# Kernel tuning notes

Measured on AMD Instinct MI355X. Metric: run time of the kernel, lower is better.

The kernel has to match this reference:

```python
import jax, jax.numpy as jnp
import numpy as np

T, B, N, IN, H, K, L = 24, 64, 207, 2, 64, 2, 2


def setup_inputs() -> dict:
    key = jax.random.key(0)
    ks = jax.random.split(key, 12)
    inputs = jax.random.normal(ks[0], (T, B, N, IN), dtype=jnp.float32)
    initial_hidden_state = jnp.zeros((L, B, N * H), dtype=jnp.float32)
    # random row-normalized support (keeps diffusion stable over the scan)
    S = jax.random.uniform(ks[1], (1, N, N), dtype=jnp.float32)
    supports = S / jnp.sum(S, axis=-1, keepdims=True)
    scale = 0.1
    return {
        "inputs": inputs,
        "initial_hidden_state": initial_hidden_state,
        "supports": supports,
        "w_gate0": scale * jax.random.normal(ks[2], ((IN + H) * (K + 1), 2 * H), dtype=jnp.float32),
        "b_gate0": jnp.ones((2 * H,), dtype=jnp.float32),
        "w_cand0": scale * jax.random.normal(ks[3], ((IN + H) * (K + 1), H), dtype=jnp.float32),
        "b_cand0": jnp.zeros((H,), dtype=jnp.float32),
        "w_gate1": scale * jax.random.normal(ks[4], ((H + H) * (K + 1), 2 * H), dtype=jnp.float32),
        "b_gate1": jnp.ones((2 * H,), dtype=jnp.float32),
        "w_cand1": scale * jax.random.normal(ks[5], ((H + H) * (K + 1), H), dtype=jnp.float32),
        "b_cand1": jnp.zeros((H,), dtype=jnp.float32),
    }


def _gconv(supports, x, w, b):
    # x: [B, N, D]; Chebyshev diffusion: x0, x1 = S@x0, x_k = 2*S@x_{k-1} - x_{k-2}
    xs = [x]
    for s in range(supports.shape[0]):
        S = supports[s]
        xk_1 = jnp.einsum('nm,bmd->bnd', S, x)
        xs.append(xk_1)
        xk_2 = x
        for _ in range(2, K + 1):
            xk = 2.0 * jnp.einsum('nm,bmd->bnd', S, xk_1) - xk_2
            xs.append(xk)
            xk_2, xk_1 = xk_1, xk
    h = jnp.concatenate(xs, axis=-1)            # [B, N, D*(K*num_supports+1)]
    return jnp.einsum('bnd,do->bno', h, w) + b


def _cell(supports, x_t, h, wg, bg, wc, bc, in_dim):
    # x_t: [B, N*in_dim], h: [B, N*H]
    bsz = x_t.shape[0]
    x = x_t.reshape(bsz, N, in_dim)
    hh = h.reshape(bsz, N, H)
    gates = jax.nn.sigmoid(_gconv(supports, jnp.concatenate([x, hh], -1), wg, bg))
    r, u = jnp.split(gates, 2, axis=-1)
    c = jnp.tanh(_gconv(supports, jnp.concatenate([x, r * hh], -1), wc, bc))
    h_new = u * hh + (1.0 - u) * c
    return h_new.reshape(bsz, N * H)


def _run_layer(supports, xs, h0, wg, bg, wc, bc, in_dim):
    def step(h, x_t):
        hn = _cell(supports, x_t, h, wg, bg, wc, bc, in_dim)
        return hn, hn
    h_last, outs = jax.lax.scan(step, h0, xs)
    return h_last, outs


def reference(inputs, initial_hidden_state, supports,
              w_gate0, b_gate0, w_cand0, b_cand0,
              w_gate1, b_gate1, w_cand1, b_cand1):
    cur = inputs.reshape(T, inputs.shape[1], -1)          # [T, B, N*IN]
    h0_last, cur = _run_layer(supports, cur, initial_hidden_state[0],
                              w_gate0, b_gate0, w_cand0, b_cand0, IN)
    h1_last, cur = _run_layer(supports, cur, initial_hidden_state[1],
                              w_gate1, b_gate1, w_cand1, b_cand1, H)
    output_hidden = jnp.stack([h0_last, h1_last], axis=0)  # [L, B, N*H]
    return output_hidden, cur                              # cur: [T, B, N*H]
```

## Files before the change

### kernel.cpp

```cpp
#include <hip/hip_runtime.h>
#include <math.h>


typedef unsigned short u16;
typedef unsigned int u32;
typedef short bf8 __attribute__((ext_vector_type(8)));
typedef float f32x4 __attribute__((ext_vector_type(4)));
typedef u16 u16x8 __attribute__((ext_vector_type(8)));

constexpr int T_ = 24, B_ = 64, N_ = 207, H_ = 64;
constexpr int BH  = 4096;
constexpr int NBH = N_ * BH;
constexpr int BNH = B_ * N_ * H_;

__device__ __forceinline__ float b2f(u16 b) {
    u32 u = ((u32)b) << 16; float f; __builtin_memcpy(&f, &u, 4); return f;
}
__device__ __forceinline__ u16 f2b(float f) {
    u32 u; __builtin_memcpy(&u, &f, 4);
    u32 r = (u + 0x7FFF + ((u >> 16) & 1)) >> 16;
    return (u16)r;
}

__global__ void s2_kernel(const float* __restrict__ S, float* __restrict__ S2) {
    const int n = blockIdx.x, m = threadIdx.x;
    if (m >= N_) return;
    float acc = 0.f;
    for (int k = 0; k < N_; ++k) acc += S[n * N_ + k] * S[k * N_ + m];
    S2[n * N_ + m] = 2.f * acc;
}

__global__ void ablk_build(const float* __restrict__ S, const float* __restrict__ S2,
                           u16* __restrict__ ablk) {
    int idx = blockIdx.x * 256 + threadIdx.x;
    if (idx >= 2 * 14 * 7 * 4 * 16 * 8) return;
    int j = idx & 7, r = (idx >> 3) & 15, kb = (idx >> 7) & 3;
    int rest = idx >> 9;
    int ks = rest % 7; rest /= 7;
    int rt = rest % 14, half = rest / 14;
    int n = rt * 16 + r, k = ks * 32 + kb * 8 + j;
    float v = 0.f;
    if (n < N_ && k < N_) v = half ? S2[n * N_ + k] : S[n * N_ + k];
    ablk[idx] = f2b(v);
}

__global__ void wblk_build(const float* __restrict__ W, u16* __restrict__ out,
                           int OF, int total, int layer) {
    int idx = blockIdx.x * 256 + threadIdx.x;
    if (idx >= total) return;
    int j = idx & 7;
    int rest = idx >> 3;
    int o = rest % OF; rest /= OF;
    int kb = rest & 3, ks = rest >> 2;
    int k = ks * 32 + kb * 8 + j;
    int blk = k >> 6, d = k & 63;
    int wrow, wsub = -1;
    if (layer == 0) {
        wrow = blk * 66 + 2 + d;
        if (blk == 0) wsub = 2 * 66 + 2 + d;
    } else {
        int sb = blk >> 1, part = blk & 1;
        wrow = sb * 128 + part * 64 + d;
        if (sb == 0) wsub = 256 + part * 64 + d;
    }
    float v = W[wrow * OF + o];
    if (wsub >= 0) v -= W[wsub * OF + o];
    out[idx] = f2b(v);
}

__global__ void wx_build(const float* __restrict__ W, float* __restrict__ out, int OF) {
    int idx = blockIdx.x * 256 + threadIdx.x;
    if (idx >= 6 * OF) return;
    int o = idx % OF, p = idx / OF;
    int cheb = p >> 1, i = p & 1;
    float v = W[(cheb * 66 + i) * OF + o];
    if (cheb == 0) v -= W[(132 + i) * OF + o];
    out[idx] = v;
}

__global__ void xt2_build(const float* __restrict__ x, u16* __restrict__ xt2) {
    int idx = blockIdx.x * 256 + threadIdx.x;
    if (idx >= N_ * T_ * B_ * 2) return;
    int i = idx & 1, b = (idx >> 1) & 63, rest = idx >> 7;
    int t = rest % T_, n = rest / T_;
    xt2[idx] = f2b(x[((t * B_ + b) * N_ + n) * 2 + i]);
}

__global__ __launch_bounds__(256) void xd_build(const float* __restrict__ S,
                                                const float* __restrict__ S2,
                                                const u16* __restrict__ xt2,
                                                u16* __restrict__ xd0,
                                                u16* __restrict__ xd1) {
    __shared__ float sS[N_], sS2[N_];
    int n = blockIdx.x;
    int c = blockIdx.y * 256 + threadIdx.x;
    for (int i = threadIdx.x; i < N_; i += 256) { sS[i] = S[n*N_+i]; sS2[i] = S2[n*N_+i]; }
    __syncthreads();
    float a1 = 0.f, a2 = 0.f;
    for (int m = 0; m < N_; ++m) {
        float xv = b2f(xt2[m * 3072 + c]);
        a1 += sS[m] * xv; a2 += sS2[m] * xv;
    }
    xd0[(size_t)n * 3072 + c] = f2b(a1);
    xd1[(size_t)n * 3072 + c] = f2b(a2);
}

__global__ void hinit_kernel(const float* __restrict__ ih, u16* __restrict__ h0b,
                             u16* __restrict__ h1b, float* __restrict__ h0f,
                             float* __restrict__ h1f) {
    int idx = blockIdx.x * 256 + threadIdx.x;
    if (idx >= NBH) return;
    int h = idx & 63, b = (idx >> 6) & 63, n = idx >> 12;
    float v0 = ih[(size_t)b * (N_ * 64) + n * 64 + h];
    float v1 = ih[(size_t)BNH + (size_t)b * (N_ * 64) + n * 64 + h];
    h0b[idx] = f2b(v0); h1b[idx] = f2b(v1);
    h0f[idx] = v0;      h1f[idx] = v1;
}

__global__ __launch_bounds__(256) void diff_kernel(
    const u16* __restrict__ ablk,
    const u16* __restrict__ srcA, const u16* __restrict__ srcB, int ctA,
    u16* __restrict__ dA1, u16* __restrict__ dA2,
    u16* __restrict__ dB1, u16* __restrict__ dB2) {
    __shared__ u16 sA[7168];
    __shared__ char sB[28672];
    const int bx = blockIdx.x, by = blockIdx.y;
    const int half = by / 7, rsub = by % 7;
    const int tid = threadIdx.x;
    const u16* src; u16* dst1; u16* dst2; int c0;
    if (bx < ctA) { src = srcA; dst1 = dA1; dst2 = dA2; c0 = bx * 64; }
    else          { src = srcB; dst1 = dB1; dst2 = dB2; c0 = (bx - ctA) * 64; }

    const u16* ga = ablk + (size_t)(half * 14 + rsub * 2) * 3584;
    for (int i = tid; i < 896; i += 256)
        *(u16x8*)(sA + i * 8) = *(const u16x8*)(ga + i * 8);

    for (int id = tid; id < 1792; id += 256) {
        int ks = id >> 8, ch = id & 255;
        int ml = ch >> 3, cc = ch & 7;
        int m = ks * 32 + ml;
        u16x8 v = {0,0,0,0,0,0,0,0};
        if (m < N_) v = *(const u16x8*)(src + (size_t)m * 4096 + c0 + cc * 8);
        *(u16x8*)(sB + ks * 4096 + ((ml * 128 + cc * 16) ^ (((ml >> 3) & 3) << 5))) = v;
    }
    __syncthreads();

    const int w = tid >> 6, lane = tid & 63, lq = lane >> 4, lr = lane & 15;
    const int rt = w & 1, cfb = (w >> 1) * 2;
    f32x4 acc[2] = {{0,0,0,0},{0,0,0,0}};
    for (int ks = 0; ks < 7; ++ks) {
        bf8 a = *(const bf8*)(sA + ((((rt * 7) + ks) * 4 + lq) * 16 + lr) * 8);
#pragma unroll
        for (int cf = 0; cf < 2; ++cf) {
            int c = (cfb + cf) * 16 + lr;
            bf8 b;
#pragma unroll
            for (int j = 0; j < 8; ++j) {
                int m = lq * 8 + j;
                b[j] = *(const short*)(sB + ks * 4096 +
                        ((m * 128 + c * 2) ^ (((m >> 3) & 3) << 5)));
            }
            acc[cf] = __builtin_amdgcn_mfma_f32_16x16x32_bf16(a, b, acc[cf], 0, 0, 0);
        }
    }
    u16* dst = half ? dst2 : dst1;
#pragma unroll
    for (int cf = 0; cf < 2; ++cf) {
        int c = c0 + (cfb + cf) * 16 + lr;
#pragma unroll
        for (int j = 0; j < 4; ++j) {
            int n = rsub * 32 + rt * 16 + lq * 4 + j;
            if (n < N_) dst[(size_t)n * 4096 + c] = f2b(acc[cf][j]);
        }
    }
}

template<int NBLK, int OF, bool XC, bool CAND, bool WCUR>
__global__ __launch_bounds__(256) void dense_kernel(
    const u16* __restrict__ s0, const u16* __restrict__ s1, const u16* __restrict__ s2v,
    const u16* __restrict__ s3, const u16* __restrict__ s4, const u16* __restrict__ s5,
    const u16* __restrict__ wblk, const float* __restrict__ bias,
    const float* __restrict__ hmul, float* __restrict__ ubuf,
    u16* __restrict__ outb, float* __restrict__ outf, float* __restrict__ cur,
    const u16* __restrict__ xt2, const u16* __restrict__ xd0,
    const u16* __restrict__ xd1, const float* __restrict__ wx, int t) {
    __shared__ char sAc[NBLK * 8192];
    const int n = blockIdx.x, oh = blockIdx.y, tid = threadIdx.x;
    const u16* const srcs[6] = {s0, s1, s2v, s3, s4, s5};
#pragma unroll
    for (int i = 0; i < NBLK; ++i) {
        const u16* sp = srcs[i] + (size_t)n * 4096;
        for (int id = tid; id < 512; id += 256) {
            int b = id >> 3, dc = id & 7;
            *(u16x8*)(sAc + i * 8192 + ((b * 128 + dc * 16) ^ ((b & 7) << 4))) =
                *(const u16x8*)(sp + b * 64 + dc * 8);
        }
    }
    __syncthreads();

    const int w = tid >> 6, lane = tid & 63, lq = lane >> 4, lr = lane & 15;
    const int ob = oh * 64;
    f32x4 acc[4] = {{0,0,0,0},{0,0,0,0},{0,0,0,0},{0,0,0,0}};
    for (int ks = 0; ks < 2 * NBLK; ++ks) {
        int blk = ks >> 1;
        int b = w * 16 + lr;
        bf8 a = *(const bf8*)(sAc + blk * 8192 +
                ((b * 128 + ((ks & 1) * 64 + lq * 16)) ^ ((b & 7) << 4)));
#pragma unroll
        for (int cf = 0; cf < 4; ++cf) {
            int o = ob + cf * 16 + lr;
            bf8 wv = *(const bf8*)(wblk + ((size_t)((ks * 4 + lq) * OF + o)) * 8);
            acc[cf] = __builtin_amdgcn_mfma_f32_16x16x32_bf16(a, wv, acc[cf], 0, 0, 0);
        }
    }

    float bv[4];
    float wxv[4][6];
#pragma unroll
    for (int cf = 0; cf < 4; ++cf) {
        bv[cf] = bias[ob + cf * 16 + lr];
        if (XC) {
#pragma unroll
            for (int p = 0; p < 6; ++p) wxv[cf][p] = wx[p * OF + ob + cf * 16 + lr];
        }
    }
#pragma unroll
    for (int j = 0; j < 4; ++j) {
        int b = w * 16 + lq * 4 + j;
        float xf[6];
        if (XC) {
            size_t cb = (size_t)n * 3072 + t * 128 + b * 2;
            xf[0] = b2f(xt2[cb]); xf[1] = b2f(xt2[cb + 1]);
            xf[2] = b2f(xd0[cb]); xf[3] = b2f(xd0[cb + 1]);
            xf[4] = b2f(xd1[cb]); xf[5] = b2f(xd1[cb + 1]);
        }
#pragma unroll
        for (int cf = 0; cf < 4; ++cf) {
            float v = acc[cf][j] + bv[cf];
            if (XC) {
#pragma unroll
                for (int p = 0; p < 6; ++p) v += xf[p] * wxv[cf][p];
            }
            int ol = cf * 16 + lr;
            size_t idx = (size_t)n * 4096 + b * 64 + ol;
            if (!CAND) {
                float g = 1.f / (1.f + __expf(-v));
                if (oh == 0) outb[idx] = f2b(g * hmul[idx]);
                else         ubuf[idx] = g;
            } else {
                float cc = tanhf(v);
                float uu = ubuf[idx];
                float hn = uu * hmul[idx] + (1.f - uu) * cc;
                outb[idx] = f2b(hn);
                outf[idx] = hn;
                if (WCUR) cur[((size_t)b * N_ + n) * 64 + ol] = hn;
            }
        }
    }
}

__global__ void final_kernel(const float* __restrict__ h0f,
                             const float* __restrict__ h1f,
                             float* __restrict__ out) {
    int idx = blockIdx.x * 256 + threadIdx.x;
    if (idx >= 2 * NBH) return;
    int l = idx / NBH, rem = idx % NBH;
    int h = rem & 63, nn = (rem >> 6) % N_, b = (rem >> 6) / N_;
    const float* src = l ? h1f : h0f;
    out[idx] = src[(size_t)nn * 4096 + b * 64 + h];
}

extern "C" void kernel_launch(void* const* d_in, const int* in_sizes, int n_in,
                              void* d_out, int out_size, void* d_ws, size_t ws_size,
                              hipStream_t stream) {
    const float* x   = (const float*)d_in[0];
    const float* ih  = (const float*)d_in[1];
    const float* S   = (const float*)d_in[2];
    const float* wg0 = (const float*)d_in[3];
    const float* bg0 = (const float*)d_in[4];
    const float* wc0 = (const float*)d_in[5];
    const float* bc0 = (const float*)d_in[6];
    const float* wg1 = (const float*)d_in[7];
    const float* bg1 = (const float*)d_in[8];
    const float* wc1 = (const float*)d_in[9];
    const float* bc1 = (const float*)d_in[10];

    char* p = (char*)d_ws;
    auto alloc = [&](size_t bytes) -> char* {
        char* r = p; p += (bytes + 255) & ~(size_t)255; return r;
    };
    float* S2    = (float*)alloc((size_t)N_ * N_ * 4);
    u16*   ablk  = (u16*)  alloc(100352 * 2);
    u16*   wg0b  = (u16*)  alloc(24576 * 2);
    u16*   wc0b  = (u16*)  alloc(12288 * 2);
    u16*   wg1b  = (u16*)  alloc(49152 * 2);
    u16*   wc1b  = (u16*)  alloc(24576 * 2);
    float* wxg0  = (float*)alloc(6 * 128 * 4);
    float* wxc0  = (float*)alloc(6 * 64 * 4);
    u16*   xt2   = (u16*)  alloc((size_t)N_ * 3072 * 2);
    u16*   xd0   = (u16*)  alloc((size_t)N_ * 3072 * 2);
    u16*   xd1   = (u16*)  alloc((size_t)N_ * 3072 * 2);
    u16*   h0init= (u16*)  alloc((size_t)NBH * 2);
    u16*   h0seq = (u16*)  alloc((size_t)T_ * NBH * 2);
    u16*   h1b   = (u16*)  alloc((size_t)NBH * 2);
    float* h0f   = (float*)alloc((size_t)NBH * 4);
    float* h1f   = (float*)alloc((size_t)NBH * 4);
    u16*   dbx1  = (u16*)  alloc((size_t)NBH * 2);
    u16*   dbx2  = (u16*)  alloc((size_t)NBH * 2);
    u16*   dbh1  = (u16*)  alloc((size_t)NBH * 2);
    u16*   dbh2  = (u16*)  alloc((size_t)NBH * 2);
    u16*   rh    = (u16*)  alloc((size_t)NBH * 2);
    float* u     = (float*)alloc((size_t)NBH * 4);

    float* out     = (float*)d_out;
    float* out_cur = out + 2 * (size_t)BNH;

    s2_kernel <<<N_, 256, 0, stream>>>(S, S2);
    ablk_build<<<392, 256, 0, stream>>>(S, S2, ablk);
    wblk_build<<<96, 256, 0, stream>>>(wg0, wg0b, 128, 24576, 0);
    wblk_build<<<48, 256, 0, stream>>>(wc0, wc0b,  64, 12288, 0);
    wblk_build<<<192, 256, 0, stream>>>(wg1, wg1b, 128, 49152, 1);
    wblk_build<<<96, 256, 0, stream>>>(wc1, wc1b,  64, 24576, 1);
    wx_build  <<<3, 256, 0, stream>>>(wg0, wxg0, 128);
    wx_build  <<<2, 256, 0, stream>>>(wc0, wxc0, 64);
    xt2_build <<<(N_ * T_ * B_ * 2 + 255) / 256, 256, 0, stream>>>(x, xt2);
    xd_build  <<<dim3(N_, 12), 256, 0, stream>>>(S, S2, xt2, xd0, xd1);
    hinit_kernel<<<(NBH + 255) / 256, 256, 0, stream>>>(ih, h0init, h1b, h0f, h1f);

    for (int t = 0; t < T_; ++t) {
        const u16* h0prevb = t ? h0seq + (size_t)(t - 1) * NBH : h0init;
        diff_kernel<<<dim3(64, 14), 256, 0, stream>>>(
            ablk, h0prevb, h0prevb, 64, dbh1, dbh2, dbh1, dbh2);
        dense_kernel<3, 128, true, false, false><<<dim3(N_, 2), 256, 0, stream>>>(
            h0prevb, dbh1, dbh2, h0prevb, h0prevb, h0prevb, wg0b, bg0,
            h0f, u, rh, nullptr, nullptr, xt2, xd0, xd1, wxg0, t);
        diff_kernel<<<dim3(64, 14), 256, 0, stream>>>(
            ablk, rh, rh, 64, dbh1, dbh2, dbh1, dbh2);
        dense_kernel<3, 64, true, true, false><<<dim3(N_, 1), 256, 0, stream>>>(
            rh, dbh1, dbh2, rh, rh, rh, wc0b, bc0,
            h0f, u, h0seq + (size_t)t * NBH, h0f, nullptr, xt2, xd0, xd1, wxc0, t);
        const u16* h0tb = h0seq + (size_t)t * NBH;
        diff_kernel<<<dim3(128, 14), 256, 0, stream>>>(
            ablk, h0tb, h1b, 64, dbx1, dbx2, dbh1, dbh2);
        dense_kernel<6, 128, false, false, false><<<dim3(N_, 2), 256, 0, stream>>>(
            h0tb, h1b, dbx1, dbh1, dbx2, dbh2, wg1b, bg1,
            h1f, u, rh, nullptr, nullptr, nullptr, nullptr, nullptr, nullptr, 0);
        diff_kernel<<<dim3(64, 14), 256, 0, stream>>>(
            ablk, rh, rh, 64, dbh1, dbh2, dbh1, dbh2);
        dense_kernel<6, 64, false, true, true><<<dim3(N_, 1), 256, 0, stream>>>(
            h0tb, rh, dbx1, dbh1, dbx2, dbh2, wc1b, bc1,
            h1f, u, h1b, h1f, out_cur + (size_t)t * BNH,
            nullptr, nullptr, nullptr, nullptr, 0);
    }

    final_kernel<<<(2 * NBH + 255) / 256, 256, 0, stream>>>(h0f, h1f, out);
}
```

Before: 2.357 ms.

## Replace per-timestep kernel launches with a single persistent DCRNN kernel

```diff
diff --git a/kernel.cpp b/kernel.cpp
--- a/kernel.cpp
+++ b/kernel.cpp
@@ -5,22 +5,25 @@
 typedef unsigned short u16;
 typedef unsigned int u32;
 typedef short bf8 __attribute__((ext_vector_type(8)));
+typedef u16 u16x4 __attribute__((ext_vector_type(4)));
+typedef u16 u16x8 __attribute__((ext_vector_type(8)));
 typedef float f32x4 __attribute__((ext_vector_type(4)));
-typedef u16 u16x8 __attribute__((ext_vector_type(8)));
 
 constexpr int T_ = 24, B_ = 64, N_ = 207, H_ = 64;
-constexpr int BH  = 4096;
-constexpr int NBH = N_ * BH;
+constexpr int NP = 224;
+constexpr int SBH = NP * H_;
 constexpr int BNH = B_ * N_ * H_;
+
+#define MFMA(a, bb, c) __builtin_amdgcn_mfma_f32_16x16x32_bf16(a, bb, c, 0, 0, 0)
 
 __device__ __forceinline__ float b2f(u16 b) {
     u32 u = ((u32)b) << 16; float f; __builtin_memcpy(&f, &u, 4); return f;
 }
 __device__ __forceinline__ u16 f2b(float f) {
     u32 u; __builtin_memcpy(&u, &f, 4);
-    u32 r = (u + 0x7FFF + ((u >> 16) & 1)) >> 16;
-    return (u16)r;
-}
+    return (u16)((u + 0x7FFF + ((u >> 16) & 1)) >> 16);
+}
+__device__ __forceinline__ float sigm(float v) { return 1.f / (1.f + __expf(-v)); }
 
 __global__ void s2_kernel(const float* __restrict__ S, float* __restrict__ S2) {
     const int n = blockIdx.x, m = threadIdx.x;
@@ -30,18 +33,21 @@
     S2[n * N_ + m] = 2.f * acc;
 }
 
-__global__ void ablk_build(const float* __restrict__ S, const float* __restrict__ S2,
-                           u16* __restrict__ ablk) {
+__global__ void sfr_build(const float* __restrict__ S, const float* __restrict__ S2,
+                          u16* __restrict__ sfr) {
     int idx = blockIdx.x * 256 + threadIdx.x;
-    if (idx >= 2 * 14 * 7 * 4 * 16 * 8) return;
-    int j = idx & 7, r = (idx >> 3) & 15, kb = (idx >> 7) & 3;
-    int rest = idx >> 9;
-    int ks = rest % 7; rest /= 7;
-    int rt = rest % 14, half = rest / 14;
-    int n = rt * 16 + r, k = ks * 32 + kb * 8 + j;
+    if (idx >= 114688) return;
+    int jj = idx & 7;
+    int tmp = idx >> 3;
+    int lane = tmp & 63; tmp >>= 6;
+    int ks = tmp % 7; tmp /= 7;
+    int rtp = tmp & 7, jb = tmp >> 3;
+    int half = rtp >> 2, rt = rtp & 3;
+    int node = jb * 52 + rt * 16 + (lane & 15);
+    int k = ks * 32 + (lane >> 4) * 8 + jj;
     float v = 0.f;
-    if (n < N_ && k < N_) v = half ? S2[n * N_ + k] : S[n * N_ + k];
-    ablk[idx] = f2b(v);
+    if (node < N_ && k < N_) v = half ? S2[node * N_ + k] : S[node * N_ + k];
+    sfr[idx] = f2b(v);
 }
 
 __global__ void wblk_build(const float* __restrict__ W, u16* __restrict__ out,
@@ -86,188 +92,352 @@
     xt2[idx] = f2b(x[((t * B_ + b) * N_ + n) * 2 + i]);
 }
 
-__global__ __launch_bounds__(256) void xd_build(const float* __restrict__ S,
-                                                const float* __restrict__ S2,
-                                                const u16* __restrict__ xt2,
-                                                u16* __restrict__ xd0,
-                                                u16* __restrict__ xd1) {
+__global__ __launch_bounds__(256) void xpack_build(const float* __restrict__ S,
+                                                   const float* __restrict__ S2,
+                                                   const u16* __restrict__ xt2,
+                                                   float* __restrict__ xpack) {
     __shared__ float sS[N_], sS2[N_];
     int n = blockIdx.x;
-    int c = blockIdx.y * 256 + threadIdx.x;
     for (int i = threadIdx.x; i < N_; i += 256) { sS[i] = S[n*N_+i]; sS2[i] = S2[n*N_+i]; }
     __syncthreads();
-    float a1 = 0.f, a2 = 0.f;
+    int c = blockIdx.y * 256 + threadIdx.x;
+    float a10 = 0, a11 = 0, a20 = 0, a21 = 0;
     for (int m = 0; m < N_; ++m) {
-        float xv = b2f(xt2[m * 3072 + c]);
-        a1 += sS[m] * xv; a2 += sS2[m] * xv;
+        float x0 = b2f(xt2[m * 3072 + c * 2]);
+        float x1 = b2f(xt2[m * 3072 + c * 2 + 1]);
+        a10 += sS[m] * x0;  a11 += sS[m] * x1;
+        a20 += sS2[m] * x0; a21 += sS2[m] * x1;
     }
-    xd0[(size_t)n * 3072 + c] = f2b(a1);
-    xd1[(size_t)n * 3072 + c] = f2b(a2);
-}
-
-__global__ void hinit_kernel(const float* __restrict__ ih, u16* __restrict__ h0b,
-                             u16* __restrict__ h1b, float* __restrict__ h0f,
-                             float* __restrict__ h1f) {
+    int t = c >> 6, bb = c & 63;
+    float* p = xpack + (size_t)((bb * 24 + t) * N_ + n) * 8;
+    p[0] = b2f(xt2[n * 3072 + c * 2]); p[1] = b2f(xt2[n * 3072 + c * 2 + 1]);
+    p[2] = a10; p[3] = a11; p[4] = a20; p[5] = a21; p[6] = 0.f; p[7] = 0.f;
+}
+
+__global__ void hinit_kernel(const float* __restrict__ ih,
+                             float* __restrict__ h0f, float* __restrict__ h1f,
+                             u16* __restrict__ mxH0, u16* __restrict__ mxH1,
+                             u16* __restrict__ xtH0, u16* __restrict__ xtH1) {
     int idx = blockIdx.x * 256 + threadIdx.x;
-    if (idx >= NBH) return;
-    int h = idx & 63, b = (idx >> 6) & 63, n = idx >> 12;
-    float v0 = ih[(size_t)b * (N_ * 64) + n * 64 + h];
-    float v1 = ih[(size_t)BNH + (size_t)b * (N_ * 64) + n * 64 + h];
-    h0b[idx] = f2b(v0); h1b[idx] = f2b(v1);
-    h0f[idx] = v0;      h1f[idx] = v1;
-}
-
-__global__ __launch_bounds__(256) void diff_kernel(
-    const u16* __restrict__ ablk,
-    const u16* __restrict__ srcA, const u16* __restrict__ srcB, int ctA,
-    u16* __restrict__ dA1, u16* __restrict__ dA2,
-    u16* __restrict__ dB1, u16* __restrict__ dB2) {
-    __shared__ u16 sA[7168];
-    __shared__ char sB[28672];
-    const int bx = blockIdx.x, by = blockIdx.y;
-    const int half = by / 7, rsub = by % 7;
+    if (idx >= BNH) return;
+    int h = idx & 63, n = (idx >> 6) % N_, b = (idx >> 6) / N_;
+    float v0 = ih[(size_t)b * 13248 + n * 64 + h];
+    float v1 = ih[(size_t)BNH + (size_t)b * 13248 + n * 64 + h];
+    size_t si = (size_t)b * SBH + n * 64 + h;
+    h0f[si] = v0; h1f[si] = v1;
+    mxH0[si] = f2b(v0); mxH1[si] = f2b(v1);
+    size_t ti = (size_t)b * SBH + h * NP + n;
+    xtH0[ti] = f2b(v0); xtH1[ti] = f2b(v1);
+}
+
+__global__ __launch_bounds__(256, 2) void dcrnn_persist(
+    const u16* __restrict__ sfr,
+    const u16* __restrict__ wg0b, const float* __restrict__ bg0, const float* __restrict__ wxg0,
+    const u16* __restrict__ wc0b, const float* __restrict__ bc0, const float* __restrict__ wxc0,
+    const u16* __restrict__ wg1b, const float* __restrict__ bg1,
+    const u16* __restrict__ wc1b, const float* __restrict__ bc1,
+    const float* __restrict__ xpack,
+    u16* __restrict__ xtH0, u16* __restrict__ xtH1,
+    u16* __restrict__ xtR0, u16* __restrict__ xtR1,
+    u16* __restrict__ mxH0, u16* __restrict__ mxH1,
+    u16* __restrict__ mxR0, u16* __restrict__ mxR1,
+    float* __restrict__ h0f, float* __restrict__ h1f,
+    u16* __restrict__ xh0d, u32* __restrict__ bar,
+    float* __restrict__ out_hid, float* __restrict__ out_cur)
+{
+    __shared__ char lds[61440];
+    char* ldsXT = lds;
+    char* xcP   = lds + 28672;
+    char* xcQ   = lds + 45056;
+
     const int tid = threadIdx.x;
-    const u16* src; u16* dst1; u16* dst2; int c0;
-    if (bx < ctA) { src = srcA; dst1 = dA1; dst2 = dA2; c0 = bx * 64; }
-    else          { src = srcB; dst1 = dB1; dst2 = dB2; c0 = (bx - ctA) * 64; }
-
-    const u16* ga = ablk + (size_t)(half * 14 + rsub * 2) * 3584;
-    for (int i = tid; i < 896; i += 256)
-        *(u16x8*)(sA + i * 8) = *(const u16x8*)(ga + i * 8);
-
-    for (int id = tid; id < 1792; id += 256) {
-        int ks = id >> 8, ch = id & 255;
-        int ml = ch >> 3, cc = ch & 7;
-        int m = ks * 32 + ml;
-        u16x8 v = {0,0,0,0,0,0,0,0};
-        if (m < N_) v = *(const u16x8*)(src + (size_t)m * 4096 + c0 + cc * 8);
-        *(u16x8*)(sB + ks * 4096 + ((ml * 128 + cc * 16) ^ (((ml >> 3) & 3) << 5))) = v;
+    const int lane = tid & 63, wid = tid >> 6;
+    const int lq = lane >> 4, lr = lane & 15;
+    const int bid = blockIdx.x;
+    const int xcd = bid & 7, qq = bid >> 3;
+    const int gin = qq >> 2, j = qq & 3;
+    const int b = xcd * 8 + gin;
+    const int nj = j * 52;
+    const int nReal = (j == 3) ? 51 : 52;
+    const size_t sb = (size_t)b * SBH;
+
+    bf8 s0[7], s1[7];
+#pragma unroll
+    for (int ks = 0; ks < 7; ++ks) {
+        s0[ks] = *(const bf8*)(sfr + (size_t)(((j * 8 + wid) * 7 + ks) * 64 + lane) * 8);
+        s1[ks] = *(const bf8*)(sfr + (size_t)(((j * 8 + 4 + wid) * 7 + ks) * 64 + lane) * 8);
     }
-    __syncthreads();
-
-    const int w = tid >> 6, lane = tid & 63, lq = lane >> 4, lr = lane & 15;
-    const int rt = w & 1, cfb = (w >> 1) * 2;
-    f32x4 acc[2] = {{0,0,0,0},{0,0,0,0}};
-    for (int ks = 0; ks < 7; ++ks) {
-        bf8 a = *(const bf8*)(sA + ((((rt * 7) + ks) * 4 + lq) * 16 + lr) * 8);
-#pragma unroll
-        for (int cf = 0; cf < 2; ++cf) {
-            int c = (cfb + cf) * 16 + lr;
-            bf8 b;
-#pragma unroll
-            for (int j = 0; j < 8; ++j) {
-                int m = lq * 8 + j;
-                b[j] = *(const short*)(sB + ks * 4096 +
-                        ((m * 128 + c * 2) ^ (((m >> 3) & 3) << 5)));
-            }
-            acc[cf] = __builtin_amdgcn_mfma_f32_16x16x32_bf16(a, b, acc[cf], 0, 0, 0);
-        }
+
+    float u0[4][4], u1[4][4];
+#pragma unroll
+    for (int a = 0; a < 4; ++a)
+#pragma unroll
+        for (int c = 0; c < 4; ++c) { u0[a][c] = 0.f; u1[a][c] = 0.f; }
+
+    u32 bar_target = 0;
+    u32* mybar = bar + b * 16;
+    auto gbar = [&]() {
+        __syncthreads();
+        __threadfence();
+        if (tid == 0)
+            __hip_atomic_fetch_add(mybar, 1u, __ATOMIC_RELEASE, __HIP_MEMORY_SCOPE_AGENT);
+        bar_target += 4;
+        while (__hip_atomic_load(mybar, __ATOMIC_ACQUIRE, __HIP_MEMORY_SCOPE_AGENT) < bar_target)
+            __builtin_amdgcn_s_sleep(2);
+        __threadfence();
+    };
+
+    auto stageXT = [&](const u16* xtg) {
+        const char* src = (const char*)(xtg + sb);
+#pragma unroll
+        for (int it = 0; it < 7; ++it) {
+            int id = it * 256 + tid;
+            int hrow = id / 28, mc = id - hrow * 28;
+            int off = hrow * 448 + mc * 16;
+            *(u16x8*)(ldsXT + (off ^ ((hrow & 7) << 4))) = *(const u16x8*)(src + off);
+        }
+    };
+
+    auto diffuse = [&](char* xc) {
+        f32x4 a0[4] = {{0,0,0,0},{0,0,0,0},{0,0,0,0},{0,0,0,0}};
+        f32x4 a1[4] = {{0,0,0,0},{0,0,0,0},{0,0,0,0},{0,0,0,0}};
+#pragma unroll
+        for (int ks = 0; ks < 7; ++ks) {
+#pragma unroll
+            for (int ct = 0; ct < 4; ++ct) {
+                int h = ct * 16 + lr;
+                bf8 Bv = *(const bf8*)(ldsXT + ((h * 448 + ks * 64 + lq * 16) ^ ((h & 7) << 4)));
+                a0[ct] = MFMA(s0[ks], Bv, a0[ct]);
+                a1[ct] = MFMA(s1[ks], Bv, a1[ct]);
+            }
+        }
+#pragma unroll
+        for (int ct = 0; ct < 4; ++ct)
+#pragma unroll
+            for (int jj = 0; jj < 4; ++jj) {
+                int row = wid * 16 + lq * 4 + jj;
+                int sw = (row & 7) << 4;
+                int k2 = (ct * 16 + lr) * 2;
+                *(u16*)(xc + ((row * 256 + k2) ^ sw))       = f2b(a0[ct][jj]);
+                *(u16*)(xc + ((row * 256 + 128 + k2) ^ sw)) = f2b(a1[ct][jj]);
+            }
+    };
+
+    auto ldW = [&](const u16* w, int OF, int ks, int o) -> bf8 {
+        return *(const bf8*)(w + (size_t)((ks * 4 + lq) * OF + o) * 8);
+    };
+    auto ldA_mx = [&](const u16* mx, int rt, int kel) -> bf8 {
+        return *(const bf8*)(mx + sb + (size_t)(nj + rt * 16 + lr) * 64 + kel);
+    };
+    auto ldA_xc = [&](const char* xc, int rt, int kel) -> bf8 {
+        int row = rt * 16 + lr;
+        return *(const bf8*)(xc + ((row * 256 + kel * 2) ^ ((row & 7) << 4)));
+    };
+    auto ldA_xh = [&](int rt, int kel) -> bf8 {
+        return *(const bf8*)(xh0d + (size_t)((b * 4 + j) * 64 + rt * 16 + lr) * 128 + kel);
+    };
+
+    char* ldsTr = ldsXT + wid * 2048;
+    auto trPut = [&](int row, float v) {
+        *(u16*)(ldsTr + ((lr * 128 + row * 2) ^ ((lr & 7) << 4))) = f2b(v);
+    };
+    auto trFlush = [&](u16* xtg, int o0) {
+        for (int it = lane; it < 208; it += 64) {
+            int ol = it / 13, r4 = it - ol * 13;
+            u16x4 v = *(const u16x4*)(ldsTr + ((ol * 128 + r4 * 8) ^ ((ol & 7) << 4)));
+            *(u16x4*)((char*)(xtg + sb) + (o0 + ol) * 448 + (nj + r4 * 4) * 2) = v;
+        }
+    };
+
+    auto saveXh = [&]() {
+        for (int it = tid; it < 1024; it += 256) {
+            int row = it >> 4, kc = it & 15;
+            u16x8 v = *(const u16x8*)(xcP + ((row * 256 + kc * 16) ^ ((row & 7) << 4)));
+            *(u16x8*)((char*)xh0d + (size_t)((b * 4 + j) * 64 + row) * 256 + kc * 16) = v;
+        }
+    };
+
+    auto dense_g0 = [&](int t) {
+        f32x4 acc[4][2] = {};
+#pragma unroll
+        for (int ks = 0; ks < 6; ++ks) {
+            bf8 W0 = ldW(wg0b, 128, ks, wid * 16 + lr);
+            bf8 W1 = ldW(wg0b, 128, ks, (wid + 4) * 16 + lr);
+#pragma unroll
+            for (int rt = 0; rt < 4; ++rt) {
+                bf8 Av = (ks < 2) ? ldA_mx(mxH0, rt, ks * 32 + lq * 8)
+                       : (ks < 4) ? ldA_xc(xcP, rt, (ks - 2) * 32 + lq * 8)
+                                  : ldA_xc(xcP, rt, 64 + (ks - 4) * 32 + lq * 8);
+                acc[rt][0] = MFMA(Av, W0, acc[rt][0]);
+                acc[rt][1] = MFMA(Av, W1, acc[rt][1]);
+            }
+        }
+        int oR = wid * 16 + lr, oU = oR + 64;
+        float wxr[6], wxu[6];
+#pragma unroll
+        for (int p = 0; p < 6; ++p) { wxr[p] = wxg0[p * 128 + oR]; wxu[p] = wxg0[p * 128 + oU]; }
+        float bR = bg0[oR], bU = bg0[oU];
+#pragma unroll
+        for (int rt = 0; rt < 4; ++rt)
+#pragma unroll
+            for (int jj = 0; jj < 4; ++jj) {
+                int row = rt * 16 + lq * 4 + jj;
+                float vR = acc[rt][0][jj] + bR, vU = acc[rt][1][jj] + bU;
+                if (row < nReal) {
+                    const float* xp = xpack + (size_t)((b * 24 + t) * N_ + nj + row) * 8;
+#pragma unroll
+                    for (int p = 0; p < 6; ++p) { vR += xp[p] * wxr[p]; vU += xp[p] * wxu[p]; }
+                }
+                float gR = sigm(vR);
+                u0[rt][jj] = sigm(vU);
+                float rh = gR * h0f[sb + (nj + row) * 64 + oR];
+                if (row < nReal) mxR0[sb + (nj + row) * 64 + oR] = f2b(rh);
+                trPut(row, rh);
+            }
+        trFlush(xtR0, wid * 16);
+    };
+
+    auto dense_g1 = [&]() {
+        f32x4 acc[4][2] = {};
+#pragma unroll
+        for (int ks = 0; ks < 12; ++ks) {
+            bf8 W0 = ldW(wg1b, 128, ks, wid * 16 + lr);
+            bf8 W1 = ldW(wg1b, 128, ks, (wid + 4) * 16 + lr);
+#pragma unroll
+            for (int rt = 0; rt < 4; ++rt) {
+                bf8 Av;
+                if (ks < 2)       Av = ldA_mx(mxH0, rt, ks * 32 + lq * 8);
+                else if (ks < 4)  Av = ldA_mx(mxH1, rt, (ks - 2) * 32 + lq * 8);
+                else if (ks < 6)  Av = ldA_xc(xcP, rt, (ks - 4) * 32 + lq * 8);
+                else if (ks < 8)  Av = ldA_xc(xcQ, rt, (ks - 6) * 32 + lq * 8);
+                else if (ks < 10) Av = ldA_xc(xcP, rt, 64 + (ks - 8) * 32 + lq * 8);
+                else              Av = ldA_xc(xcQ, rt, 64 + (ks - 10) * 32 + lq * 8);
+                acc[rt][0] = MFMA(Av, W0, acc[rt][0]);
+                acc[rt][1] = MFMA(Av, W1, acc[rt][1]);
+            }
+        }
+        int oR = wid * 16 + lr, oU = oR + 64;
+        float bR = bg1[oR], bU = bg1[oU];
+#pragma unroll
+        for (int rt = 0; rt < 4; ++rt)
+#pragma unroll
+            for (int jj = 0; jj < 4; ++jj) {
+                int row = rt * 16 + lq * 4 + jj;
+                float gR = sigm(acc[rt][0][jj] + bR);
+                u1[rt][jj] = sigm(acc[rt][1][jj] + bU);
+                float rh = gR * h1f[sb + (nj + row) * 64 + oR];
+                if (row < nReal) mxR1[sb + (nj + row) * 64 + oR] = f2b(rh);
+                trPut(row, rh);
+            }
+        trFlush(xtR1, wid * 16);
+    };
+
+    auto dense_c1 = [&](int w) {
+        int t1 = w - 1;
+        f32x4 acc[4] = {};
+#pragma unroll
+        for (int ks = 0; ks < 12; ++ks) {
+            bf8 Wv = ldW(wc1b, 64, ks, wid * 16 + lr);
+#pragma unroll
+            for (int rt = 0; rt < 4; ++rt) {
+                bf8 Av;
+                if (ks < 2)       Av = ldA_mx(mxH0, rt, ks * 32 + lq * 8);
+                else if (ks < 4)  Av = ldA_mx(mxR1, rt, (ks - 2) * 32 + lq * 8);
+                else if (ks < 6)  Av = ldA_xh(rt, (ks - 4) * 32 + lq * 8);
+                else if (ks < 8)  Av = ldA_xc(xcQ, rt, (ks - 6) * 32 + lq * 8);
+                else if (ks < 10) Av = ldA_xh(rt, 64 + (ks - 8) * 32 + lq * 8);
+                else              Av = ldA_xc(xcQ, rt, 64 + (ks - 10) * 32 + lq * 8);
+                acc[rt] = MFMA(Av, Wv, acc[rt]);
+            }
+        }
+        int o = wid * 16 + lr;
+        float bv = bc1[o];
+#pragma unroll
+        for (int rt = 0; rt < 4; ++rt)
+#pragma unroll
+            for (int jj = 0; jj < 4; ++jj) {
+                int row = rt * 16 + lq * 4 + jj;
+                int n = nj + row;
+                float cv = tanhf(acc[rt][jj] + bv);
+                float hold = h1f[sb + n * 64 + o];
+                float hn = u1[rt][jj] * hold + (1.f - u1[rt][jj]) * cv;
+                if (row < nReal) {
+                    h1f[sb + n * 64 + o] = hn;
+                    mxH1[sb + n * 64 + o] = f2b(hn);
+                    out_cur[(size_t)((t1 * 64 + b) * N_ + n) * 64 + o] = hn;
+                }
+                trPut(row, hn);
+            }
+        trFlush(xtH1, wid * 16);
+    };
+
+    auto dense_c0 = [&](int t) {
+        f32x4 acc[4] = {};
+#pragma unroll
+        for (int ks = 0; ks < 6; ++ks) {
+            bf8 Wv = ldW(wc0b, 64, ks, wid * 16 + lr);
+#pragma unroll
+            for (int rt = 0; rt < 4; ++rt) {
+                bf8 Av = (ks < 2) ? ldA_mx(mxR0, rt, ks * 32 + lq * 8)
+                       : (ks < 4) ? ldA_xc(xcP, rt, (ks - 2) * 32 + lq * 8)
+                                  : ldA_xc(xcP, rt, 64 + (ks - 4) * 32 + lq * 8);
+                acc[rt] = MFMA(Av, Wv, acc[rt]);
+            }
+        }
+        int o = wid * 16 + lr;
+        float bv = bc0[o];
+        float wxc[6];
+#pragma unroll
+        for (int p = 0; p < 6; ++p) wxc[p] = wxc0[p * 64 + o];
+#pragma unroll
+        for (int rt = 0; rt < 4; ++rt)
+#pragma unroll
+            for (int jj = 0; jj < 4; ++jj) {
+                int row = rt * 16 + lq * 4 + jj;
+                int n = nj + row;
+                float v = acc[rt][jj] + bv;
+                if (row < nReal) {
+                    const float* xp = xpack + (size_t)((b * 24 + t) * N_ + n) * 8;
+#pragma unroll
+                    for (int p = 0; p < 6; ++p) v += xp[p] * wxc[p];
+                }
+                float cv = tanhf(v);
+                float hold = h0f[sb + n * 64 + o];
+                float hn = u0[rt][jj] * hold + (1.f - u0[rt][jj]) * cv;
+                if (row < nReal) {
+                    h0f[sb + n * 64 + o] = hn;
+                    mxH0[sb + n * 64 + o] = f2b(hn);
+                }
+                trPut(row, hn);
+            }
+        trFlush(xtH0, wid * 16);
+    };
+
+    for (int w = 0; w <= 24; ++w) {
+        const bool L0 = (w < 24), L1 = (w >= 1);
+        gbar();
+        stageXT(xtH0); __syncthreads();
+        diffuse(xcP);  __syncthreads();
+        if (L1) { stageXT(xtH1); __syncthreads(); diffuse(xcQ); }
+        __syncthreads();
+        saveXh();
+        if (L0) dense_g0(w);
+        if (L1) dense_g1();
+        gbar();
+        if (L0) { stageXT(xtR0); __syncthreads(); diffuse(xcP); __syncthreads(); }
+        if (L1) { stageXT(xtR1); __syncthreads(); diffuse(xcQ); }
+        __syncthreads();
+        if (L1) dense_c1(w);
+        __syncthreads();
+        if (L0) dense_c0(w);
     }
-    u16* dst = half ? dst2 : dst1;
-#pragma unroll
-    for (int cf = 0; cf < 2; ++cf) {
-        int c = c0 + (cfb + cf) * 16 + lr;
-#pragma unroll
-        for (int j = 0; j < 4; ++j) {
-            int n = rsub * 32 + rt * 16 + lq * 4 + j;
-            if (n < N_) dst[(size_t)n * 4096 + c] = f2b(acc[cf][j]);
-        }
+
+    for (int it = tid; it < nReal * 64; it += 256) {
+        int row = it >> 6, h = it & 63;
+        int n = nj + row;
+        out_hid[(size_t)b * 13248 + n * 64 + h] = h0f[sb + n * 64 + h];
+        out_hid[(size_t)BNH + (size_t)b * 13248 + n * 64 + h] = h1f[sb + n * 64 + h];
     }
-}
-
-template<int NBLK, int OF, bool XC, bool CAND, bool WCUR>
-__global__ __launch_bounds__(256) void dense_kernel(
-    const u16* __restrict__ s0, const u16* __restrict__ s1, const u16* __restrict__ s2v,
-    const u16* __restrict__ s3, const u16* __restrict__ s4, const u16* __restrict__ s5,
-    const u16* __restrict__ wblk, const float* __restrict__ bias,
-    const float* __restrict__ hmul, float* __restrict__ ubuf,
-    u16* __restrict__ outb, float* __restrict__ outf, float* __restrict__ cur,
-    const u16* __restrict__ xt2, const u16* __restrict__ xd0,
-    const u16* __restrict__ xd1, const float* __restrict__ wx, int t) {
-    __shared__ char sAc[NBLK * 8192];
-    const int n = blockIdx.x, oh = blockIdx.y, tid = threadIdx.x;
-    const u16* const srcs[6] = {s0, s1, s2v, s3, s4, s5};
-#pragma unroll
-    for (int i = 0; i < NBLK; ++i) {
-        const u16* sp = srcs[i] + (size_t)n * 4096;
-        for (int id = tid; id < 512; id += 256) {
-            int b = id >> 3, dc = id & 7;
-            *(u16x8*)(sAc + i * 8192 + ((b * 128 + dc * 16) ^ ((b & 7) << 4))) =
-                *(const u16x8*)(sp + b * 64 + dc * 8);
-        }
-    }
-    __syncthreads();
-
-    const int w = tid >> 6, lane = tid & 63, lq = lane >> 4, lr = lane & 15;
-    const int ob = oh * 64;
-    f32x4 acc[4] = {{0,0,0,0},{0,0,0,0},{0,0,0,0},{0,0,0,0}};
-    for (int ks = 0; ks < 2 * NBLK; ++ks) {
-        int blk = ks >> 1;
-        int b = w * 16 + lr;
-        bf8 a = *(const bf8*)(sAc + blk * 8192 +
-                ((b * 128 + ((ks & 1) * 64 + lq * 16)) ^ ((b & 7) << 4)));
-#pragma unroll
-        for (int cf = 0; cf < 4; ++cf) {
-            int o = ob + cf * 16 + lr;
-            bf8 wv = *(const bf8*)(wblk + ((size_t)((ks * 4 + lq) * OF + o)) * 8);
-            acc[cf] = __builtin_amdgcn_mfma_f32_16x16x32_bf16(a, wv, acc[cf], 0, 0, 0);
-        }
-    }
-
-    float bv[4];
-    float wxv[4][6];
-#pragma unroll
-    for (int cf = 0; cf < 4; ++cf) {
-        bv[cf] = bias[ob + cf * 16 + lr];
-        if (XC) {
-#pragma unroll
-            for (int p = 0; p < 6; ++p) wxv[cf][p] = wx[p * OF + ob + cf * 16 + lr];
-        }
-    }
-#pragma unroll
-    for (int j = 0; j < 4; ++j) {
-        int b = w * 16 + lq * 4 + j;
-        float xf[6];
-        if (XC) {
-            size_t cb = (size_t)n * 3072 + t * 128 + b * 2;
-            xf[0] = b2f(xt2[cb]); xf[1] = b2f(xt2[cb + 1]);
-            xf[2] = b2f(xd0[cb]); xf[3] = b2f(xd0[cb + 1]);
-            xf[4] = b2f(xd1[cb]); xf[5] = b2f(xd1[cb + 1]);
-        }
-#pragma unroll
-        for (int cf = 0; cf < 4; ++cf) {
-            float v = acc[cf][j] + bv[cf];
-            if (XC) {
-#pragma unroll
-                for (int p = 0; p < 6; ++p) v += xf[p] * wxv[cf][p];
-            }
-            int ol = cf * 16 + lr;
-            size_t idx = (size_t)n * 4096 + b * 64 + ol;
-            if (!CAND) {
-                float g = 1.f / (1.f + __expf(-v));
-                if (oh == 0) outb[idx] = f2b(g * hmul[idx]);
-                else         ubuf[idx] = g;
-            } else {
-                float cc = tanhf(v);
-                float uu = ubuf[idx];
-                float hn = uu * hmul[idx] + (1.f - uu) * cc;
-                outb[idx] = f2b(hn);
-                outf[idx] = hn;
-                if (WCUR) cur[((size_t)b * N_ + n) * 64 + ol] = hn;
-            }
-        }
-    }
-}
-
-__global__ void final_kernel(const float* __restrict__ h0f,
-                             const float* __restrict__ h1f,
-                             float* __restrict__ out) {
-    int idx = blockIdx.x * 256 + threadIdx.x;
-    if (idx >= 2 * NBH) return;
-    int l = idx / NBH, rem = idx % NBH;
-    int h = rem & 63, nn = (rem >> 6) % N_, b = (rem >> 6) / N_;
-    const float* src = l ? h1f : h0f;
-    out[idx] = src[(size_t)nn * 4096 + b * 64 + h];
 }
 
 extern "C" void kernel_launch(void* const* d_in, const int* in_sizes, int n_in,
@@ -290,7 +460,7 @@
         char* r = p; p += (bytes + 255) & ~(size_t)255; return r;
     };
     float* S2    = (float*)alloc((size_t)N_ * N_ * 4);
-    u16*   ablk  = (u16*)  alloc(100352 * 2);
+    u16*   sfr   = (u16*)  alloc(114688 * 2);
     u16*   wg0b  = (u16*)  alloc(24576 * 2);
     u16*   wc0b  = (u16*)  alloc(12288 * 2);
     u16*   wg1b  = (u16*)  alloc(49152 * 2);
@@ -298,60 +468,40 @@
     float* wxg0  = (float*)alloc(6 * 128 * 4);
     float* wxc0  = (float*)alloc(6 * 64 * 4);
     u16*   xt2   = (u16*)  alloc((size_t)N_ * 3072 * 2);
-    u16*   xd0   = (u16*)  alloc((size_t)N_ * 3072 * 2);
-    u16*   xd1   = (u16*)  alloc((size_t)N_ * 3072 * 2);
-    u16*   h0init= (u16*)  alloc((size_t)NBH * 2);
-    u16*   h0seq = (u16*)  alloc((size_t)T_ * NBH * 2);
-    u16*   h1b   = (u16*)  alloc((size_t)NBH * 2);
-    float* h0f   = (float*)alloc((size_t)NBH * 4);
-    float* h1f   = (float*)alloc((size_t)NBH * 4);
-    u16*   dbx1  = (u16*)  alloc((size_t)NBH * 2);
-    u16*   dbx2  = (u16*)  alloc((size_t)NBH * 2);
-    u16*   dbh1  = (u16*)  alloc((size_t)NBH * 2);
-    u16*   dbh2  = (u16*)  alloc((size_t)NBH * 2);
-    u16*   rh    = (u16*)  alloc((size_t)NBH * 2);
-    float* u     = (float*)alloc((size_t)NBH * 4);
+    float* xpack = (float*)alloc((size_t)64 * 24 * N_ * 8 * 4);
+    u16*   xtH0  = (u16*)  alloc((size_t)B_ * SBH * 2);
+    u16*   xtH1  = (u16*)  alloc((size_t)B_ * SBH * 2);
+    u16*   xtR0  = (u16*)  alloc((size_t)B_ * SBH * 2);
+    u16*   xtR1  = (u16*)  alloc((size_t)B_ * SBH * 2);
+    u16*   mxH0  = (u16*)  alloc((size_t)B_ * SBH * 2);
+    u16*   mxH1  = (u16*)  alloc((size_t)B_ * SBH * 2);
+    u16*   mxR0  = (u16*)  alloc((size_t)B_ * SBH * 2);
+    u16*   mxR1  = (u16*)  alloc((size_t)B_ * SBH * 2);
+    float* h0f   = (float*)alloc((size_t)B_ * SBH * 4);
+    float* h1f   = (float*)alloc((size_t)B_ * SBH * 4);
+    u16*   xh0d  = (u16*)  alloc((size_t)B_ * 4 * 64 * 128 * 2);
+    u32*   bar   = (u32*)  alloc(64 * 64);
 
     float* out     = (float*)d_out;
     float* out_cur = out + 2 * (size_t)BNH;
 
-    s2_kernel <<<N_, 256, 0, stream>>>(S, S2);
-    ablk_build<<<392, 256, 0, stream>>>(S, S2, ablk);
-    wblk_build<<<96, 256, 0, stream>>>(wg0, wg0b, 128, 24576, 0);
-    wblk_build<<<48, 256, 0, stream>>>(wc0, wc0b,  64, 12288, 0);
-    wblk_build<<<192, 256, 0, stream>>>(wg1, wg1b, 128, 49152, 1);
-    wblk_build<<<96, 256, 0, stream>>>(wc1, wc1b,  64, 24576, 1);
-    wx_build  <<<3, 256, 0, stream>>>(wg0, wxg0, 128);
-    wx_build  <<<2, 256, 0, stream>>>(wc0, wxc0, 64);
-    xt2_build <<<(N_ * T_ * B_ * 2 + 255) / 256, 256, 0, stream>>>(x, xt2);
-    xd_build  <<<dim3(N_, 12), 256, 0, stream>>>(S, S2, xt2, xd0, xd1);
-    hinit_kernel<<<(NBH + 255) / 256, 256, 0, stream>>>(ih, h0init, h1b, h0f, h1f);
-
-    for (int t = 0; t < T_; ++t) {
-        const u16* h0prevb = t ? h0seq + (size_t)(t - 1) * NBH : h0init;
-        diff_kernel<<<dim3(64, 14), 256, 0, stream>>>(
-            ablk, h0prevb, h0prevb, 64, dbh1, dbh2, dbh1, dbh2);
-        dense_kernel<3, 128, true, false, false><<<dim3(N_, 2), 256, 0, stream>>>(
-            h0prevb, dbh1, dbh2, h0prevb, h0prevb, h0prevb, wg0b, bg0,
-            h0f, u, rh, nullptr, nullptr, xt2, xd0, xd1, wxg0, t);
-        diff_kernel<<<dim3(64, 14), 256, 0, stream>>>(
-            ablk, rh, rh, 64, dbh1, dbh2, dbh1, dbh2);
-        dense_kernel<3, 64, true, true, false><<<dim3(N_, 1), 256, 0, stream>>>(
-            rh, dbh1, dbh2, rh, rh, rh, wc0b, bc0,
-            h0f, u, h0seq + (size_t)t * NBH, h0f, nullptr, xt2, xd0, xd1, wxc0, t);
-        const u16* h0tb = h0seq + (size_t)t * NBH;
-        diff_kernel<<<dim3(128, 14), 256, 0, stream>>>(
-            ablk, h0tb, h1b, 64, dbx1, dbx2, dbh1, dbh2);
-        dense_kernel<6, 128, false, false, false><<<dim3(N_, 2), 256, 0, stream>>>(
-            h0tb, h1b, dbx1, dbh1, dbx2, dbh2, wg1b, bg1,
-            h1f, u, rh, nullptr, nullptr, nullptr, nullptr, nullptr, nullptr, 0);
-        diff_kernel<<<dim3(64, 14), 256, 0, stream>>>(
-            ablk, rh, rh, 64, dbh1, dbh2, dbh1, dbh2);
-        dense_kernel<6, 64, false, true, true><<<dim3(N_, 1), 256, 0, stream>>>(
-            h0tb, rh, dbx1, dbh1, dbx2, dbh2, wc1b, bc1,
-            h1f, u, h1b, h1f, out_cur + (size_t)t * BNH,
-            nullptr, nullptr, nullptr, nullptr, 0);
-    }
-
-    final_kernel<<<(2 * NBH + 255) / 256, 256, 0, stream>>>(h0f, h1f, out);
-}
+    hipMemsetAsync(xtH0, 0, (size_t)8 * B_ * SBH * 2, stream);
+    hipMemsetAsync(bar, 0, 64 * 64, stream);
+
+    s2_kernel  <<<N_, 256, 0, stream>>>(S, S2);
+    sfr_build  <<<448, 256, 0, stream>>>(S, S2, sfr);
+    wblk_build <<<96,  256, 0, stream>>>(wg0, wg0b, 128, 24576, 0);
+    wblk_build <<<48,  256, 0, stream>>>(wc0, wc0b,  64, 12288, 0);
+    wblk_build <<<192, 256, 0, stream>>>(wg1, wg1b, 128, 49152, 1);
+    wblk_build <<<96,  256, 0, stream>>>(wc1, wc1b,  64, 24576, 1);
+    wx_build   <<<3, 256, 0, stream>>>(wg0, wxg0, 128);
+    wx_build   <<<2, 256, 0, stream>>>(wc0, wxc0, 64);
+    xt2_build  <<<2484, 256, 0, stream>>>(x, xt2);
+    xpack_build<<<dim3(N_, 6), 256, 0, stream>>>(S, S2, xt2, xpack);
+    hinit_kernel<<<(BNH + 255) / 256, 256, 0, stream>>>(ih, h0f, h1f, mxH0, mxH1, xtH0, xtH1);
+
+    dcrnn_persist<<<256, 256, 0, stream>>>(
+        sfr, wg0b, bg0, wxg0, wc0b, bc0, wxc0, wg1b, bg1, wc1b, bc1,
+        xpack, xtH0, xtH1, xtR0, xtR1, mxH0, mxH1, mxR0, mxR1,
+        h0f, h1f, xh0d, bar, out, out_cur);
+}
```

Result: slower. 6.763 ms (+187.0%).
